# Optimization experiments

Hardware: AMD Instinct MI355X
Metric: run time of the kernel (lower is better)

## Reference

```python
import jax, jax.numpy as jnp
import numpy as np

B, D, T, H = 2048, 512, 16, 1024   # batch, covariate_dim, treatment_dim, mlp hidden
K, M = 50, 16                       # k_neighbors, manifold_dim


def _mlp(xt, W1, b1, W2, b2):
    # outcome model: [B, D+T] -> [B, 1]
    return jnp.tanh(xt @ W1 + b1) @ W2 + b2


def setup_inputs() -> dict:
    key = jax.random.key(0)
    k0, k1, k2, k3, k4 = jax.random.split(key, 5)
    x = jax.random.normal(k0, (B, D), dtype=jnp.float32)
    t = jax.random.normal(k1, (B, T), dtype=jnp.float32)
    perturbations = jax.random.normal(k2, (B, D), dtype=jnp.float32)
    W1 = jax.random.normal(k3, (D + T, H), dtype=jnp.float32) / np.float32(np.sqrt(D + T))
    b1 = jnp.zeros((H,), dtype=jnp.float32)
    W2 = jax.random.normal(k4, (H, 1), dtype=jnp.float32) / np.float32(np.sqrt(H))
    b2 = jnp.zeros((1,), dtype=jnp.float32)
    return {"x": x, "t": t, "perturbations": perturbations,
            "W1": W1, "b1": b1, "W2": W2, "b2": b2}


def reference(x, t, perturbations, W1, b1, W2, b2):
    # grad of sum(y) w.r.t. x (create_graph analog handled by composing jax.grad)
    def scalar_out(xx):
        return _mlp(jnp.concatenate([xx, t], axis=-1), W1, b1, W2, b2).sum()
    grad_x = jax.grad(scalar_out)(x)                      # [B, D]

    # kNN on perturbations (squared distances preserve topk-smallest ordering)
    sq = jnp.sum(perturbations * perturbations, axis=-1)  # [B]
    d2 = sq[:, None] + sq[None, :] - 2.0 * (perturbations @ perturbations.T)
    _, idx = jax.lax.top_k(-d2, K)                        # [B, K] nearest (incl. self)

    neigh = perturbations[idx]                            # [B, K, D] gather
    centered = neigh - neigh.mean(axis=1, keepdims=True)
    # batched reduced SVD: Vt has shape [B, min(K,D), D]
    _, _, Vt = jnp.linalg.svd(centered, full_matrices=False)
    basis = jnp.swapaxes(Vt[:, :M, :], 1, 2)              # [B, D, M] top-M right sing. vecs

    # projection of grad onto tangent space, summed squared norm
    coef = jnp.einsum('bdm,bd->bm', basis, grad_x)        # [B, M]
    proj = jnp.einsum('bdm,bm->bd', basis, coef)          # [B, D]
    return jnp.sum(proj * proj) / B
```

## Files before the change

kernel.cpp:

```cpp
#include <hip/hip_runtime.h>
#include <math.h>
#include <float.h>

#define B_ 2048
#define D_ 512
#define T_ 16
#define H_ 1024
#define K_ 50
#define M_ 16
#define NSWEEP 1
#define SX_STRIDE 2656
#define SLAB 128
#define SROW 136
#define FS 52

typedef __attribute__((ext_vector_type(8))) short s16x8;
typedef __attribute__((ext_vector_type(4))) float f32x4;
typedef __attribute__((ext_vector_type(2))) float f32x2;

#define GLL16(g, l) __builtin_amdgcn_global_load_lds( \
    (const __attribute__((address_space(1))) void*)(g), \
    (__attribute__((address_space(3))) void*)(l), 16, 0, 0)

__device__ __forceinline__ float bsum64(float v) {
  #pragma unroll
  for (int o = 1; o < 64; o <<= 1) v += __shfl_xor(v, o);
  return v;
}

__device__ __forceinline__ unsigned bf16_rne(float v) {
  union { float f; unsigned u; } a; a.f = v;
  return (a.u + 0x7FFFu + ((a.u >> 16) & 1u)) >> 16;
}
__device__ __forceinline__ float bf16_val(unsigned h) {
  union { unsigned u; float f; } a; a.u = h << 16;
  return a.f;
}
__device__ __forceinline__ void split_bf16(float v, unsigned short* h, unsigned short* l) {
  unsigned hh = bf16_rne(v);
  *h = (unsigned short)hh;
  *l = (unsigned short)bf16_rne(v - bf16_val(hh));
}

__global__ __launch_bounds__(256)
void prep_conv(const float* __restrict__ x, const float* __restrict__ t,
               const float* __restrict__ P, const float* __restrict__ W1,
               unsigned short* __restrict__ xh, unsigned short* __restrict__ xl,
               unsigned short* __restrict__ ph, unsigned short* __restrict__ pl,
               float* __restrict__ sq,
               unsigned short* __restrict__ th, unsigned short* __restrict__ tl,
               unsigned short* __restrict__ wh, unsigned short* __restrict__ wl,
               float* __restrict__ out) {
  __shared__ float tile[32][33];
  __shared__ float red[4];
  const int bid = blockIdx.x, tid = threadIdx.x;
  if (bid < B_) {
    const int b = bid;
    if (b == 0 && tid == 0) out[0] = 0.f;
    for (int c = tid; c < 544; c += 256) {
      float v = 0.f;
      if (c < 512) v = x[(size_t)b * 512 + c];
      else if (c < 528) v = t[(size_t)b * 16 + (c - 512)];
      unsigned short hh, ll; split_bf16(v, &hh, &ll);
      xh[(size_t)b * 544 + c] = hh;
      xl[(size_t)b * 544 + c] = ll;
    }
    float s = 0.f;
    for (int c = tid; c < 512; c += 256) {
      float v = P[(size_t)b * 512 + c];
      s += v * v;
      unsigned short hh, ll; split_bf16(v, &hh, &ll);
      ph[(size_t)b * 512 + c] = hh;
      pl[(size_t)b * 512 + c] = ll;
    }
    s = bsum64(s);
    if ((tid & 63) == 0) red[tid >> 6] = s;
    __syncthreads();
    if (tid == 0) sq[b] = (red[0] + red[1]) + (red[2] + red[3]);
  } else {
    const int cid = bid - B_;
    const int tx = tid & 31, ty = tid >> 5;
    const int kb = (cid % 17) * 32, hb = (cid / 17) * 32;
    #pragma unroll
    for (int j = 0; j < 4; j++) {
      int k = kb + ty + j * 8;
      float v = (k < 528) ? W1[(size_t)k * 1024 + hb + tx] : 0.f;
      tile[ty + j * 8][tx] = v;
      if (k < 528) {
        unsigned short hh, ll; split_bf16(v, &hh, &ll);
        wh[(size_t)k * 1024 + hb + tx] = hh;
        wl[(size_t)k * 1024 + hb + tx] = ll;
      }
    }
    __syncthreads();
    #pragma unroll
    for (int j = 0; j < 4; j++) {
      int hrow = hb + ty + j * 8;
      float v = tile[tx][ty + j * 8];
      unsigned short hh, ll; split_bf16(v, &hh, &ll);
      th[(size_t)hrow * 544 + kb + tx] = hh;
      tl[(size_t)hrow * 544 + kb + tx] = ll;
    }
  }
}

template <int EPI, int PASSES>
__global__ __launch_bounds__(256)
void mfma_nt(const unsigned short* __restrict__ Ah, const unsigned short* __restrict__ Al, int lda,
             const unsigned short* __restrict__ Bh, const unsigned short* __restrict__ Bl, int ldb,
             int K, float* __restrict__ C, int ldc,
             const float* __restrict__ b1, const float* __restrict__ W2,
             unsigned short* __restrict__ acth, unsigned short* __restrict__ actl) {
  __shared__ unsigned short sAh[2 * 2048], sBh[2 * 2048];
  __shared__ unsigned short sAl[PASSES == 3 ? 2 * 2048 : 16];
  __shared__ unsigned short sBl[PASSES == 3 ? 2 * 2048 : 16];
  const int tid = threadIdx.x;
  const int lane = tid & 63, wv = tid >> 6;
  const int wm = wv >> 1, wn = wv & 1;
  const int lr = lane & 15, lq = lane >> 4;
  const int m0 = blockIdx.y * 64, n0 = blockIdx.x * 64;
  const int srow = wv * 16 + (lane >> 2);
  const int sx = (srow & 3) ^ ((srow >> 2) & 3);
  const int gch = ((lane & 3) ^ sx) * 8;
  const size_t rowA = (size_t)(m0 + srow) * lda + gch;
  const size_t rowB = (size_t)(n0 + srow) * ldb + gch;

  f32x4 acc[2][2];
  #pragma unroll
  for (int mt = 0; mt < 2; mt++)
    #pragma unroll
    for (int nt = 0; nt < 2; nt++)
      #pragma unroll
      for (int i = 0; i < 4; i++) acc[mt][nt][i] = 0.f;

  auto STAGE = [&](int bufi, int kb) {
    const int off = bufi * 2048 + wv * 512;
    GLL16(Ah + rowA + kb, &sAh[off]);
    GLL16(Bh + rowB + kb, &sBh[off]);
    if (PASSES == 3) {
      GLL16(Al + rowA + kb, &sAl[off]);
      GLL16(Bl + rowB + kb, &sBl[off]);
    }
  };

  auto COMPUTE = [&](int bufi) {
    const int bo = bufi * 2048;
    s16x8 fah[2], fal[2], fbh[2], fbl[2];
    #pragma unroll
    for (int mt = 0; mt < 2; mt++) {
      const int r = wm * 32 + mt * 16 + lr;
      const int xo = (lq ^ ((r & 3) ^ ((r >> 2) & 3))) * 8;
      fah[mt] = *(const s16x8*)&sAh[bo + r * 32 + xo];
      if (PASSES == 3) fal[mt] = *(const s16x8*)&sAl[bo + r * 32 + xo];
    }
    #pragma unroll
    for (int nt = 0; nt < 2; nt++) {
      const int r = wn * 32 + nt * 16 + lr;
      const int xo = (lq ^ ((r & 3) ^ ((r >> 2) & 3))) * 8;
      fbh[nt] = *(const s16x8*)&sBh[bo + r * 32 + xo];
      if (PASSES == 3) fbl[nt] = *(const s16x8*)&sBl[bo + r * 32 + xo];
    }
    #pragma unroll
    for (int mt = 0; mt < 2; mt++)
      #pragma unroll
      for (int nt = 0; nt < 2; nt++)
        acc[mt][nt] = __builtin_amdgcn_mfma_f32_16x16x32_bf16(fah[mt], fbh[nt], acc[mt][nt], 0, 0, 0);
    if (PASSES == 3) {
      #pragma unroll
      for (int mt = 0; mt < 2; mt++)
        #pragma unroll
        for (int nt = 0; nt < 2; nt++)
          acc[mt][nt] = __builtin_amdgcn_mfma_f32_16x16x32_bf16(fah[mt], fbl[nt], acc[mt][nt], 0, 0, 0);
      #pragma unroll
      for (int mt = 0; mt < 2; mt++)
        #pragma unroll
        for (int nt = 0; nt < 2; nt++)
          acc[mt][nt] = __builtin_amdgcn_mfma_f32_16x16x32_bf16(fal[mt], fbh[nt], acc[mt][nt], 0, 0, 0);
    }
  };

  STAGE(0, 0);
  __syncthreads();
  int cur = 0;
  for (int kb = 32; kb < K; kb += 32) {
    STAGE(cur ^ 1, kb);
    COMPUTE(cur);
    __syncthreads();
    cur ^= 1;
  }
  COMPUTE(cur);

  #pragma unroll
  for (int nt = 0; nt < 2; nt++) {
    const int n = n0 + wn * 32 + nt * 16 + lr;
    float bb = 0.f, ww = 0.f;
    if (EPI == 1) { bb = b1[n]; ww = W2[n]; }
    #pragma unroll
    for (int mt = 0; mt < 2; mt++) {
      #pragma unroll
      for (int r = 0; r < 4; r++) {
        const int m = m0 + wm * 32 + mt * 16 + lq * 4 + r;
        float v = acc[mt][nt][r];
        if (EPI == 0) {
          C[(size_t)m * ldc + n] = v;
        } else if (EPI == 1) {
          float z = v + bb;
          float e = __builtin_amdgcn_exp2f(fabsf(z) * -2.885390082f);
          float rc = __builtin_amdgcn_rcpf(1.f + e);
          float s = 4.f * e * rc * rc * ww;
          unsigned short hh, ll; split_bf16(s, &hh, &ll);
          acth[(size_t)m * ldc + n] = hh;
          actl[(size_t)m * ldc + n] = ll;
        } else {
          unsigned short hh, ll; split_bf16(v, &hh, &ll);
          acth[(size_t)m * ldc + n] = hh;
          actl[(size_t)m * ldc + n] = ll;
        }
      }
    }
  }
}

__global__ __launch_bounds__(256)
void sbuild_kernel(const unsigned short* __restrict__ ph, const unsigned short* __restrict__ pl,
                   const unsigned short* __restrict__ gh, const unsigned short* __restrict__ gl,
                   const int* __restrict__ idx, float* __restrict__ Sx) {
  __shared__ unsigned short sh[64 * SROW];
  __shared__ unsigned short sl[64 * SROW];
  __shared__ int ids[K_];
  const int b = blockIdx.x;
  const int tid = threadIdx.x;
  if (tid < K_) ids[tid] = idx[b * K_ + tid];
  const int lane = tid & 63, wv = tid >> 6;
  const int wm = wv >> 1, wn = wv & 1;
  const int lr = lane & 15, lq = lane >> 4;
  const int strow = tid >> 4, stk = (tid & 15) * 8;
  __syncthreads();

  f32x4 acc[2][2];
  #pragma unroll
  for (int mt = 0; mt < 2; mt++)
    #pragma unroll
    for (int nt = 0; nt < 2; nt++)
      #pragma unroll
      for (int i = 0; i < 4; i++) acc[mt][nt][i] = 0.f;

  for (int kb = 0; kb < 512; kb += SLAB) {
    __syncthreads();
    #pragma unroll
    for (int p = 0; p < 4; p++) {
      const int r = p * 16 + strow;
      if (r < 51) {
        const unsigned short* srch = (r < 50) ? ph + (size_t)ids[r] * 512 : gh + (size_t)b * 512;
        const unsigned short* srcl = (r < 50) ? pl + (size_t)ids[r] * 512 : gl + (size_t)b * 512;
        *(float4*)&sh[r * SROW + stk] = *(const float4*)(srch + kb + stk);
        *(float4*)&sl[r * SROW + stk] = *(const float4*)(srcl + kb + stk);
      }
    }
    __syncthreads();
    #pragma unroll
    for (int kk = 0; kk < SLAB; kk += 32) {
      s16x8 fah[2], fal[2], fbh[2], fbl[2];
      #pragma unroll
      for (int mt = 0; mt < 2; mt++) {
        const int r = wm * 32 + mt * 16 + lr;
        fah[mt] = *(const s16x8*)&sh[r * SROW + kk + lq * 8];
        fal[mt] = *(const s16x8*)&sl[r * SROW + kk + lq * 8];
      }
      #pragma unroll
      for (int nt = 0; nt < 2; nt++) {
        const int r = wn * 32 + nt * 16 + lr;
        fbh[nt] = *(const s16x8*)&sh[r * SROW + kk + lq * 8];
        fbl[nt] = *(const s16x8*)&sl[r * SROW + kk + lq * 8];
      }
      #pragma unroll
      for (int mt = 0; mt < 2; mt++)
        #pragma unroll
        for (int nt = 0; nt < 2; nt++)
          acc[mt][nt] = __builtin_amdgcn_mfma_f32_16x16x32_bf16(fah[mt], fbh[nt], acc[mt][nt], 0, 0, 0);
      #pragma unroll
      for (int mt = 0; mt < 2; mt++)
        #pragma unroll
        for (int nt = 0; nt < 2; nt++)
          acc[mt][nt] = __builtin_amdgcn_mfma_f32_16x16x32_bf16(fah[mt], fbl[nt], acc[mt][nt], 0, 0, 0);
      #pragma unroll
      for (int mt = 0; mt < 2; mt++)
        #pragma unroll
        for (int nt = 0; nt < 2; nt++)
          acc[mt][nt] = __builtin_amdgcn_mfma_f32_16x16x32_bf16(fal[mt], fbh[nt], acc[mt][nt], 0, 0, 0);
    }
  }

  float* Sb = Sx + (size_t)b * SX_STRIDE;
  #pragma unroll
  for (int nt = 0; nt < 2; nt++) {
    const int n = wn * 32 + nt * 16 + lr;
    #pragma unroll
    for (int mt = 0; mt < 2; mt++) {
      #pragma unroll
      for (int r = 0; r < 4; r++) {
        const int m = wm * 32 + mt * 16 + lq * 4 + r;
        if (m < 51 && n < 52) Sb[m * 52 + n] = acc[mt][nt][r];
      }
    }
  }
}

__device__ __forceinline__ unsigned fkey(float f) {
  unsigned u = __float_as_uint(f);
  return u ^ ((unsigned)((int)u >> 31) | 0x80000000u);
}

__global__ __launch_bounds__(64)
void topk_kernel(const float* __restrict__ G, const float* __restrict__ sq,
                 int* __restrict__ idx) {
  const int b = blockIdx.x, lane = threadIdx.x;
  const float* row = G + (size_t)b * 2048;
  unsigned k[32];
  #pragma unroll
  for (int i = 0; i < 32; i++) {
    const int j = i * 64 + lane;
    k[i] = fkey(sq[j] - 2.f * row[j]);
  }
  unsigned V = 0;
  bool exact = false;
  for (int bit = 31; bit >= 0; bit--) {
    const unsigned cand = V | (1u << bit);
    int cnt = 0;
    #pragma unroll
    for (int i = 0; i < 32; i++) cnt += (k[i] < cand) ? 1 : 0;
    #pragma unroll
    for (int o = 1; o < 64; o <<= 1) cnt += __shfl_xor(cnt, o);
    if (cnt == K_) { V = cand; exact = true; break; }
    if (cnt < K_ + 1) V = cand;
  }
  int base = 0;
  #pragma unroll
  for (int i = 0; i < 32; i++) {
    const bool p = (k[i] < V);
    const unsigned long long mask = __ballot(p);
    if (p) {
      const int pos = base + __popcll(mask & ((1ull << lane) - 1ull));
      idx[b * K_ + pos] = i * 64 + lane;
    }
    base += __popcll(mask);
  }
  if (!exact && base < K_) {
    #pragma unroll
    for (int i = 0; i < 32; i++) {
      if (base >= K_) break;
      const bool p = (k[i] == V);
      const unsigned long long mask = __ballot(p);
      if (p) {
        const int pos = base + __popcll(mask & ((1ull << lane) - 1ull));
        if (pos < K_) idx[b * K_ + pos] = i * 64 + lane;
      }
      base += __popcll(mask);
    }
  }
}

__global__ __launch_bounds__(64, 4)
void final_kernel(const float* __restrict__ Sx, float* __restrict__ out) {
  __shared__ float cols[K_ * FS];
  const int b = blockIdx.x;
  const int lane = threadIdx.x;
  const float* Sb = Sx + (size_t)b * SX_STRIDE;
  const bool act = lane < K_;

  float q = act ? Sb[50 * 52 + lane] : 0.f;
  float qm = bsum64(q) * (1.f / K_);
  float w = act ? (q - qm) : 0.f;

  f32x2 f2[25];
  #pragma unroll
  for (int i = 0; i < 25; i++) {
    f2[i].x = act ? Sb[(2 * i) * 52 + lane] : 0.f;
    f2[i].y = act ? Sb[(2 * i + 1) * 52 + lane] : 0.f;
  }

  float cm = 0.f;
  #pragma unroll
  for (int i = 0; i < 25; i++) cm += f2[i].x + f2[i].y;
  cm *= (1.f / K_);
  float gs = bsum64(act ? cm : 0.f) * (1.f / K_);
  float cs = cm - gs;
  #pragma unroll
  for (int i = 0; i < 25; i++) {
    float r0 = __shfl(cm, 2 * i);
    float r1 = __shfl(cm, 2 * i + 1);
    if (act) { f2[i].x -= r0 + cs; f2[i].y -= r1 + cs; }
  }

  float nrm = 0.f;
  #pragma unroll
  for (int i = 0; i < 25; i++) nrm += f2[i].x * f2[i].x + f2[i].y * f2[i].y;

  f32x4 f4[13];
  #pragma unroll
  for (int k = 0; k < 12; k++) {
    f4[k].x = f2[2 * k].x;     f4[k].y = f2[2 * k].y;
    f4[k].z = f2[2 * k + 1].x; f4[k].w = f2[2 * k + 1].y;
  }
  f4[12].x = f2[24].x; f4[12].y = f2[24].y; f4[12].z = nrm; f4[12].w = w;

  float* my = &cols[lane * FS];
  if (act) {
    #pragma unroll
    for (int k = 0; k < 13; k++) *(f32x4*)&my[4 * k] = f4[k];
  }

  for (int sweep = 0; sweep < NSWEEP; sweep++) {
    int mm = (lane == 0) ? 0 : 49 - lane;
    int kkv = 0;
    for (int r = 0; r < 49; r++) {
      if (act) {
        int m = mm;
        if (lane == kkv) m = 49;
        if (lane == 49)  m = kkv;

        const float* pc = &cols[m * FS];
        f32x4 y4[13];
        #pragma unroll
        for (int k = 0; k < 13; k++) y4[k] = *(const f32x4*)&pc[4 * k];
        const float onrm = y4[12].z;
        const float yw   = y4[12].w;

        f32x4 acc4 = {0.f, 0.f, 0.f, 0.f};
        #pragma unroll
        for (int k = 0; k < 12; k++) acc4 = __builtin_elementwise_fma(f4[k], y4[k], acc4);
        acc4.x = fmaf(f4[12].x, y4[12].x, acc4.x);
        acc4.y = fmaf(f4[12].y, y4[12].y, acc4.y);
        const float dot = (acc4.x + acc4.y) + (acc4.z + acc4.w);

        const bool isp = lane < m;
        float alpha = isp ? nrm : onrm;
        float beta  = isp ? onrm : nrm;
        float tau = (beta - alpha) * 0.5f * __builtin_amdgcn_rcpf(dot);
        float sg = (tau >= 0.f) ? 1.f : -1.f;
        float s1 = __builtin_amdgcn_sqrtf(1.f + tau * tau);
        float tt = sg * __builtin_amdgcn_rcpf(fabsf(tau) + s1);
        float cc = __builtin_amdgcn_rsqf(1.f + tt * tt);
        float ssv = tt * cc;
        float sr = isp ? -ssv : ssv;
        if (fabsf(dot) < 1e-20f) { cc = 1.f; sr = 0.f; }

        f32x4 c4 = {cc, cc, cc, cc};
        f32x4 s4 = {sr, sr, sr, sr};
        #pragma unroll
        for (int k = 0; k < 13; k++)
          f4[k] = __builtin_elementwise_fma(c4, f4[k], s4 * y4[k]);
        w = cc * w + sr * yw;
        nrm = cc * cc * nrm + sr * sr * onrm + 2.f * cc * sr * dot;
        f4[12].z = nrm;
        f4[12].w = w;

        #pragma unroll
        for (int k = 0; k < 13; k++) *(f32x4*)&my[4 * k] = f4[k];
      }
      mm = (mm == 48) ? 0 : mm + 1;
      kkv += 25; if (kkv >= 49) kkv -= 49;
    }
  }

  float n2 = 0.f;
  #pragma unroll
  for (int k = 0; k < 12; k++)
    n2 += f4[k].x * f4[k].x + f4[k].y * f4[k].y + f4[k].z * f4[k].z + f4[k].w * f4[k].w;
  n2 += f4[12].x * f4[12].x + f4[12].y * f4[12].y;
  int rank = 0;
  #pragma unroll
  for (int j = 0; j < K_; j++) {
    float vj = __shfl(n2, j);
    rank += (vj > n2 || (vj == n2 && j < lane)) ? 1 : 0;
  }
  float lam = sqrtf(n2);
  float contrib = (act && rank < M_) ? (w * w / lam) : 0.f;
  contrib = bsum64(contrib);
  if (lane == 0) atomicAdd(out, contrib * (1.f / B_));
}

extern "C" void kernel_launch(void* const* d_in, const int* in_sizes, int n_in,
                              void* d_out, int out_size, void* d_ws, size_t ws_size,
                              hipStream_t stream) {
  const float* x  = (const float*)d_in[0];
  const float* t  = (const float*)d_in[1];
  const float* P  = (const float*)d_in[2];
  const float* W1 = (const float*)d_in[3];
  const float* b1 = (const float*)d_in[4];
  const float* W2 = (const float*)d_in[5];
  float* out = (float*)d_out;

  float* G    = (float*)d_ws;
  float* Sx   = (float*)d_ws;
  unsigned short* xt_h  = (unsigned short*)(G + (size_t)B_ * B_);
  unsigned short* xt_l  = xt_h  + (size_t)B_ * 544;
  unsigned short* w1t_h = xt_l  + (size_t)B_ * 544;
  unsigned short* w1t_l = w1t_h + (size_t)H_ * 544;
  unsigned short* w1_h  = w1t_l + (size_t)H_ * 544;
  unsigned short* w1_l  = w1_h  + (size_t)528 * H_;
  unsigned short* p_h   = w1_l  + (size_t)528 * H_;
  unsigned short* p_l   = p_h   + (size_t)B_ * D_;
  unsigned short* act_h = p_l   + (size_t)B_ * D_;
  unsigned short* act_l = act_h + (size_t)B_ * H_;
  unsigned short* g_h   = act_l + (size_t)B_ * H_;
  unsigned short* g_l   = g_h   + (size_t)B_ * D_;
  float* sq   = (float*)(g_l + (size_t)B_ * D_);
  int*   idx  = (int*)(sq + B_);

  prep_conv<<<B_ + 544, 256, 0, stream>>>(x, t, P, W1, xt_h, xt_l, p_h, p_l, sq,
                                          w1t_h, w1t_l, w1_h, w1_l, out);

  mfma_nt<1, 3><<<dim3(H_ / 64, B_ / 64), 256, 0, stream>>>(
      xt_h, xt_l, 544, w1t_h, w1t_l, 544, 544,
      nullptr, H_, b1, W2, act_h, act_l);
  mfma_nt<2, 3><<<dim3(D_ / 64, B_ / 64), 256, 0, stream>>>(
      act_h, act_l, H_, w1_h, w1_l, H_, H_,
      nullptr, D_, nullptr, nullptr, g_h, g_l);
  mfma_nt<0, 1><<<dim3(B_ / 64, B_ / 64), 256, 0, stream>>>(
      p_h, nullptr, D_, p_h, nullptr, D_, D_,
      G, B_, nullptr, nullptr, nullptr, nullptr);

  topk_kernel<<<B_, 64, 0, stream>>>(G, sq, idx);
  sbuild_kernel<<<B_, 256, 0, stream>>>(p_h, p_l, g_h, g_l, idx, Sx);
  final_kernel<<<B_, 64, 0, stream>>>(Sx, out);
}
```

Before: 261.3 us.

## Fuse independent GEMMs into one launch and merge topk/sbuild/final into tail kernel

Combines the first MLP GEMM and the Gram-matrix GEMM into a single grid dispatched by block index so both run concurrently, and launches the gradient GEMM separately. Topk selection, the neighbour Gram build, and the Jacobi/eigen finalisation are merged into one per-batch kernel that keeps indices and the 51x52 matrix in shared memory. This removes launch overhead and the global round-trips for idx and Sx. The trade-off is larger shared memory per block with a smaller slab of 64, and three idle waves during the serial topk and Jacobi phases.

Result: slower. 316.5 us (+21.2%).

```diff
diff --git a/kernel.cpp b/kernel.cpp
--- a/kernel.cpp
+++ b/kernel.cpp
@@ -9,9 +9,8 @@
 #define K_ 50
 #define M_ 16
 #define NSWEEP 1
-#define SX_STRIDE 2656
-#define SLAB 128
-#define SROW 136
+#define SLAB2 64
+#define SROW2 72
 #define FS 52
 
 typedef __attribute__((ext_vector_type(8))) short s16x8;
@@ -105,20 +104,19 @@
 }
 
 template <int EPI, int PASSES>
-__global__ __launch_bounds__(256)
-void mfma_nt(const unsigned short* __restrict__ Ah, const unsigned short* __restrict__ Al, int lda,
-             const unsigned short* __restrict__ Bh, const unsigned short* __restrict__ Bl, int ldb,
-             int K, float* __restrict__ C, int ldc,
-             const float* __restrict__ b1, const float* __restrict__ W2,
-             unsigned short* __restrict__ acth, unsigned short* __restrict__ actl) {
-  __shared__ unsigned short sAh[2 * 2048], sBh[2 * 2048];
-  __shared__ unsigned short sAl[PASSES == 3 ? 2 * 2048 : 16];
-  __shared__ unsigned short sBl[PASSES == 3 ? 2 * 2048 : 16];
+__device__ __forceinline__
+void gemm_tile(const unsigned short* __restrict__ Ah, const unsigned short* __restrict__ Al, int lda,
+               const unsigned short* __restrict__ Bh, const unsigned short* __restrict__ Bl, int ldb,
+               int K, float* __restrict__ C, int ldc,
+               const float* __restrict__ b1, const float* __restrict__ W2,
+               unsigned short* __restrict__ acth, unsigned short* __restrict__ actl,
+               int m0, int n0,
+               unsigned short* sAh, unsigned short* sBh,
+               unsigned short* sAl, unsigned short* sBl) {
   const int tid = threadIdx.x;
   const int lane = tid & 63, wv = tid >> 6;
   const int wm = wv >> 1, wn = wv & 1;
   const int lr = lane & 15, lq = lane >> 4;
-  const int m0 = blockIdx.y * 64, n0 = blockIdx.x * 64;
   const int srow = wv * 16 + (lane >> 2);
   const int sx = (srow & 3) ^ ((srow >> 2) & 3);
   const int gch = ((lane & 3) ^ sx) * 8;
@@ -222,20 +220,107 @@
 }
 
 __global__ __launch_bounds__(256)
-void sbuild_kernel(const unsigned short* __restrict__ ph, const unsigned short* __restrict__ pl,
-                   const unsigned short* __restrict__ gh, const unsigned short* __restrict__ gl,
-                   const int* __restrict__ idx, float* __restrict__ Sx) {
-  __shared__ unsigned short sh[64 * SROW];
-  __shared__ unsigned short sl[64 * SROW];
+void gemm_actG(const unsigned short* __restrict__ xt_h, const unsigned short* __restrict__ xt_l,
+               const unsigned short* __restrict__ w1t_h, const unsigned short* __restrict__ w1t_l,
+               const float* __restrict__ b1, const float* __restrict__ W2,
+               unsigned short* __restrict__ act_h, unsigned short* __restrict__ act_l,
+               const unsigned short* __restrict__ p_h, float* __restrict__ G) {
+  __shared__ unsigned short sAh[2 * 2048], sBh[2 * 2048];
+  __shared__ unsigned short sAl[2 * 2048], sBl[2 * 2048];
+  const int bid = blockIdx.x;
+  if (bid < 512) {
+    const int n0 = (bid & 15) * 64, m0 = (bid >> 4) * 64;
+    gemm_tile<1, 3>(xt_h, xt_l, 544, w1t_h, w1t_l, 544, 544,
+                    nullptr, H_, b1, W2, act_h, act_l, m0, n0,
+                    sAh, sBh, sAl, sBl);
+  } else {
+    const int idx = bid - 512;
+    const int n0 = (idx & 31) * 64, m0 = (idx >> 5) * 64;
+    gemm_tile<0, 1>(p_h, nullptr, D_, p_h, nullptr, D_, D_,
+                    G, B_, nullptr, nullptr, nullptr, nullptr, m0, n0,
+                    sAh, sBh, sAl, sBl);
+  }
+}
+
+__global__ __launch_bounds__(256)
+void mfma_grad(const unsigned short* __restrict__ act_h, const unsigned short* __restrict__ act_l,
+               const unsigned short* __restrict__ w1_h, const unsigned short* __restrict__ w1_l,
+               unsigned short* __restrict__ g_h, unsigned short* __restrict__ g_l) {
+  __shared__ unsigned short sAh[2 * 2048], sBh[2 * 2048];
+  __shared__ unsigned short sAl[2 * 2048], sBl[2 * 2048];
+  const int n0 = (blockIdx.x & 7) * 64, m0 = (blockIdx.x >> 3) * 64;
+  gemm_tile<2, 3>(act_h, act_l, H_, w1_h, w1_l, H_, H_,
+                  nullptr, D_, nullptr, nullptr, g_h, g_l, m0, n0,
+                  sAh, sBh, sAl, sBl);
+}
+
+__device__ __forceinline__ unsigned fkey(float f) {
+  unsigned u = __float_as_uint(f);
+  return u ^ ((unsigned)((int)u >> 31) | 0x80000000u);
+}
+
+__global__ __launch_bounds__(256)
+void tail_kernel(const float* __restrict__ G, const float* __restrict__ sq,
+                 const unsigned short* __restrict__ ph, const unsigned short* __restrict__ pl,
+                 const unsigned short* __restrict__ gh, const unsigned short* __restrict__ gl,
+                 float* __restrict__ out) {
+  __shared__ float smemf[4608];
   __shared__ int ids[K_];
-  const int b = blockIdx.x;
-  const int tid = threadIdx.x;
-  if (tid < K_) ids[tid] = idx[b * K_ + tid];
+  unsigned short* sh = (unsigned short*)smemf;
+  unsigned short* sl = ((unsigned short*)smemf) + 64 * SROW2;
+  const int b = blockIdx.x, tid = threadIdx.x;
   const int lane = tid & 63, wv = tid >> 6;
+
+  if (wv == 0) {
+    const float* row = G + (size_t)b * 2048;
+    unsigned k[32];
+    #pragma unroll
+    for (int i = 0; i < 32; i++) {
+      const int j = i * 64 + lane;
+      k[i] = fkey(sq[j] - 2.f * row[j]);
+    }
+    unsigned V = 0;
+    bool exact = false;
+    for (int bit = 31; bit >= 0; bit--) {
+      const unsigned cand = V | (1u << bit);
+      int cnt = 0;
+      #pragma unroll
+      for (int i = 0; i < 32; i++) cnt += (k[i] < cand) ? 1 : 0;
+      #pragma unroll
+      for (int o = 1; o < 64; o <<= 1) cnt += __shfl_xor(cnt, o);
+      if (cnt == K_) { V = cand; exact = true; break; }
+      if (cnt < K_ + 1) V = cand;
+    }
+    int base = 0;
+    #pragma unroll
+    for (int i = 0; i < 32; i++) {
+      const bool p = (k[i] < V);
+      const unsigned long long mask = __ballot(p);
+      if (p) {
+        const int pos = base + __popcll(mask & ((1ull << lane) - 1ull));
+        ids[pos] = i * 64 + lane;
+      }
+      base += __popcll(mask);
+    }
+    if (!exact && base < K_) {
+      #pragma unroll
+      for (int i = 0; i < 32; i++) {
+        if (base >= K_) break;
+        const bool p = (k[i] == V);
+        const unsigned long long mask = __ballot(p);
+        if (p) {
+          const int pos = base + __popcll(mask & ((1ull << lane) - 1ull));
+          if (pos < K_) ids[pos] = i * 64 + lane;
+        }
+        base += __popcll(mask);
+      }
+    }
+  }
+  __syncthreads();
+
   const int wm = wv >> 1, wn = wv & 1;
   const int lr = lane & 15, lq = lane >> 4;
-  const int strow = tid >> 4, stk = (tid & 15) * 8;
-  __syncthreads();
+  const int strow = tid >> 3, stk = (tid & 7) * 8;
 
   f32x4 acc[2][2];
   #pragma unroll
@@ -245,33 +330,33 @@
       #pragma unroll
       for (int i = 0; i < 4; i++) acc[mt][nt][i] = 0.f;
 
-  for (int kb = 0; kb < 512; kb += SLAB) {
+  for (int kb = 0; kb < 512; kb += SLAB2) {
     __syncthreads();
     #pragma unroll
-    for (int p = 0; p < 4; p++) {
-      const int r = p * 16 + strow;
+    for (int p = 0; p < 2; p++) {
+      const int r = p * 32 + strow;
       if (r < 51) {
         const unsigned short* srch = (r < 50) ? ph + (size_t)ids[r] * 512 : gh + (size_t)b * 512;
         const unsigned short* srcl = (r < 50) ? pl + (size_t)ids[r] * 512 : gl + (size_t)b * 512;
-        *(float4*)&sh[r * SROW + stk] = *(const float4*)(srch + kb + stk);
-        *(float4*)&sl[r * SROW + stk] = *(const float4*)(srcl + kb + stk);
+        *(float4*)&sh[r * SROW2 + stk] = *(const float4*)(srch + kb + stk);
+        *(float4*)&sl[r * SROW2 + stk] = *(const float4*)(srcl + kb + stk);
       }
     }
     __syncthreads();
     #pragma unroll
-    for (int kk = 0; kk < SLAB; kk += 32) {
+    for (int kk = 0; kk < SLAB2; kk += 32) {
       s16x8 fah[2], fal[2], fbh[2], fbl[2];
       #pragma unroll
       for (int mt = 0; mt < 2; mt++) {
         const int r = wm * 32 + mt * 16 + lr;
-        fah[mt] = *(const s16x8*)&sh[r * SROW + kk + lq * 8];
-        fal[mt] = *(const s16x8*)&sl[r * SROW + kk + lq * 8];
+        fah[mt] = *(const s16x8*)&sh[r * SROW2 + kk + lq * 8];
+        fal[mt] = *(const s16x8*)&sl[r * SROW2 + kk + lq * 8];
       }
       #pragma unroll
       for (int nt = 0; nt < 2; nt++) {
         const int r = wn * 32 + nt * 16 + lr;
-        fbh[nt] = *(const s16x8*)&sh[r * SROW + kk + lq * 8];
-        fbl[nt] = *(const s16x8*)&sl[r * SROW + kk + lq * 8];
+        fbh[nt] = *(const s16x8*)&sh[r * SROW2 + kk + lq * 8];
+        fbl[nt] = *(const s16x8*)&sl[r * SROW2 + kk + lq * 8];
       }
       #pragma unroll
       for (int mt = 0; mt < 2; mt++)
@@ -291,7 +376,7 @@
     }
   }
 
-  float* Sb = Sx + (size_t)b * SX_STRIDE;
+  __syncthreads();
   #pragma unroll
   for (int nt = 0; nt < 2; nt++) {
     const int n = wn * 32 + nt * 16 + lr;
@@ -300,83 +385,24 @@
       #pragma unroll
       for (int r = 0; r < 4; r++) {
         const int m = wm * 32 + mt * 16 + lq * 4 + r;
-        if (m < 51 && n < 52) Sb[m * 52 + n] = acc[mt][nt][r];
-      }
-    }
-  }
-}
-
-__device__ __forceinline__ unsigned fkey(float f) {
-  unsigned u = __float_as_uint(f);
-  return u ^ ((unsigned)((int)u >> 31) | 0x80000000u);
-}
-
-__global__ __launch_bounds__(64)
-void topk_kernel(const float* __restrict__ G, const float* __restrict__ sq,
-                 int* __restrict__ idx) {
-  const int b = blockIdx.x, lane = threadIdx.x;
-  const float* row = G + (size_t)b * 2048;
-  unsigned k[32];
-  #pragma unroll
-  for (int i = 0; i < 32; i++) {
-    const int j = i * 64 + lane;
-    k[i] = fkey(sq[j] - 2.f * row[j]);
-  }
-  unsigned V = 0;
-  bool exact = false;
-  for (int bit = 31; bit >= 0; bit--) {
-    const unsigned cand = V | (1u << bit);
-    int cnt = 0;
-    #pragma unroll
-    for (int i = 0; i < 32; i++) cnt += (k[i] < cand) ? 1 : 0;
-    #pragma unroll
-    for (int o = 1; o < 64; o <<= 1) cnt += __shfl_xor(cnt, o);
-    if (cnt == K_) { V = cand; exact = true; break; }
-    if (cnt < K_ + 1) V = cand;
-  }
-  int base = 0;
-  #pragma unroll
-  for (int i = 0; i < 32; i++) {
-    const bool p = (k[i] < V);
-    const unsigned long long mask = __ballot(p);
-    if (p) {
-      const int pos = base + __popcll(mask & ((1ull << lane) - 1ull));
-      idx[b * K_ + pos] = i * 64 + lane;
-    }
-    base += __popcll(mask);
-  }
-  if (!exact && base < K_) {
-    #pragma unroll
-    for (int i = 0; i < 32; i++) {
-      if (base >= K_) break;
-      const bool p = (k[i] == V);
-      const unsigned long long mask = __ballot(p);
-      if (p) {
-        const int pos = base + __popcll(mask & ((1ull << lane) - 1ull));
-        if (pos < K_) idx[b * K_ + pos] = i * 64 + lane;
-      }
-      base += __popcll(mask);
-    }
-  }
-}
-
-__global__ __launch_bounds__(64, 4)
-void final_kernel(const float* __restrict__ Sx, float* __restrict__ out) {
-  __shared__ float cols[K_ * FS];
-  const int b = blockIdx.x;
-  const int lane = threadIdx.x;
-  const float* Sb = Sx + (size_t)b * SX_STRIDE;
+        if (m < 51 && n < 52) smemf[m * 52 + n] = acc[mt][nt][r];
+      }
+    }
+  }
+  __syncthreads();
+
+  if (wv != 0) return;
   const bool act = lane < K_;
 
-  float q = act ? Sb[50 * 52 + lane] : 0.f;
+  float q = act ? smemf[50 * 52 + lane] : 0.f;
   float qm = bsum64(q) * (1.f / K_);
   float w = act ? (q - qm) : 0.f;
 
   f32x2 f2[25];
   #pragma unroll
   for (int i = 0; i < 25; i++) {
-    f2[i].x = act ? Sb[(2 * i) * 52 + lane] : 0.f;
-    f2[i].y = act ? Sb[(2 * i + 1) * 52 + lane] : 0.f;
+    f2[i].x = act ? smemf[(2 * i) * 52 + lane] : 0.f;
+    f2[i].y = act ? smemf[(2 * i + 1) * 52 + lane] : 0.f;
   }
 
   float cm = 0.f;
@@ -404,7 +430,7 @@
   }
   f4[12].x = f2[24].x; f4[12].y = f2[24].y; f4[12].z = nrm; f4[12].w = w;
 
-  float* my = &cols[lane * FS];
+  float* my = &smemf[lane * FS];
   if (act) {
     #pragma unroll
     for (int k = 0; k < 13; k++) *(f32x4*)&my[4 * k] = f4[k];
@@ -419,7 +445,7 @@
         if (lane == kkv) m = 49;
         if (lane == 49)  m = kkv;
 
-        const float* pc = &cols[m * FS];
+        const float* pc = &smemf[m * FS];
         f32x4 y4[13];
         #pragma unroll
         for (int k = 0; k < 13; k++) y4[k] = *(const f32x4*)&pc[4 * k];
@@ -492,7 +518,6 @@
   float* out = (float*)d_out;
 
   float* G    = (float*)d_ws;
-  float* Sx   = (float*)d_ws;
   unsigned short* xt_h  = (unsigned short*)(G + (size_t)B_ * B_);
   unsigned short* xt_l  = xt_h  + (size_t)B_ * 544;
   unsigned short* w1t_h = xt_l  + (size_t)B_ * 544;
@@ -506,22 +531,14 @@
   unsigned short* g_h   = act_l + (size_t)B_ * H_;
   unsigned short* g_l   = g_h   + (size_t)B_ * D_;
   float* sq   = (float*)(g_l + (size_t)B_ * D_);
-  int*   idx  = (int*)(sq + B_);
 
   prep_conv<<<B_ + 544, 256, 0, stream>>>(x, t, P, W1, xt_h, xt_l, p_h, p_l, sq,
                                           w1t_h, w1t_l, w1_h, w1_l, out);
 
-  mfma_nt<1, 3><<<dim3(H_ / 64, B_ / 64), 256, 0, stream>>>(
-      xt_h, xt_l, 544, w1t_h, w1t_l, 544, 544,
-      nullptr, H_, b1, W2, act_h, act_l);
-  mfma_nt<2, 3><<<dim3(D_ / 64, B_ / 64), 256, 0, stream>>>(
-      act_h, act_l, H_, w1_h, w1_l, H_, H_,
-      nullptr, D_, nullptr, nullptr, g_h, g_l);
-  mfma_nt<0, 1><<<dim3(B_ / 64, B_ / 64), 256, 0, stream>>>(
-      p_h, nullptr, D_, p_h, nullptr, D_, D_,
-      G, B_, nullptr, nullptr, nullptr, nullptr);
-
-  topk_kernel<<<B_, 64, 0, stream>>>(G, sq, idx);
-  sbuild_kernel<<<B_, 256, 0, stream>>>(p_h, p_l, g_h, g_l, idx, Sx);
-  final_kernel<<<B_, 64, 0, stream>>>(Sx, out);
-}
+  gemm_actG<<<1536, 256, 0, stream>>>(xt_h, xt_l, w1t_h, w1t_l, b1, W2,
+                                      act_h, act_l, p_h, G);
+
+  mfma_grad<<<256, 256, 0, stream>>>(act_h, act_l, w1_h, w1_l, g_h, g_l);
+
+  tail_kernel<<<B_, 256, 0, stream>>>(G, sq, p_h, p_l, g_h, g_l, out);
+}
```
